# Optimization experiments

Measured on AMD Instinct MI355X. Metric: run time of the kernel, lower is better.

## Reference

```python
import jax, jax.numpy as jnp
import numpy as np

N_NODES = 10000
D_IN = 128
D_OUT = 128
N_EDGES = 640000


def setup_inputs() -> dict:
    key = jax.random.key(0)
    k_x, k_e, k_wl, k_wr, k_b = jax.random.split(key, 5)
    x = jax.random.normal(k_x, (N_NODES, D_IN), dtype=jnp.float32)
    edge_index = jax.random.randint(k_e, (2, N_EDGES), 0, N_NODES, dtype=jnp.int64)
    # SAGEConv params: lin_l (neighbor path, with bias), lin_r (root path, no bias)
    s_l = 1.0 / np.sqrt(D_IN)
    W_l = jax.random.uniform(k_wl, (D_OUT, D_IN), dtype=jnp.float32, minval=-s_l, maxval=s_l)
    b_l = jax.random.uniform(k_b, (D_OUT,), dtype=jnp.float32, minval=-s_l, maxval=s_l)
    W_r = jax.random.uniform(k_wr, (D_OUT, D_IN), dtype=jnp.float32, minval=-s_l, maxval=s_l)
    return {"x": x, "edge_index": edge_index, "W_l": W_l, "b_l": b_l, "W_r": W_r}


def reference(x, edge_index, W_l, b_l, W_r):
    x = x.astype(jnp.float32)
    src, dst = edge_index[0], edge_index[1]
    # gather source features, mean-aggregate into destination nodes
    msgs = x[src]                                   # [E, D_in] irregular gather
    agg_sum = jax.ops.segment_sum(msgs, dst, num_segments=N_NODES)  # [N, D_in]
    deg = jax.ops.segment_sum(jnp.ones((src.shape[0],), dtype=x.dtype), dst,
                              num_segments=N_NODES)                 # [N]
    agg = jnp.where(deg[:, None] > 0, agg_sum / jnp.maximum(deg, 1.0)[:, None], 0.0)
    # SAGEConv: lin_l(agg) + lin_r(x)
    y = agg @ W_l.T + b_l + x @ W_r.T               # [N, D_out]
    return x + y                                     # residual add
```

## Files before the change

### kernel.cpp

```cpp
#include <hip/hip_runtime.h>

#define N_NODES 10000
#define D 128
#define N_EDGES 640000
#define NB 256
#define EPB (N_EDGES / NB)
#define SB 40
#define NPSB 250

typedef __attribute__((ext_vector_type(8))) short bf16x8;
typedef __attribute__((ext_vector_type(4))) float f32x4;
typedef __attribute__((ext_vector_type(8))) unsigned short us8;
typedef __attribute__((ext_vector_type(8))) float f32x8;


__device__ __forceinline__ unsigned short f2bf(float f) {
    union { float f; unsigned int i; } v;
    v.f = f;
    unsigned int b = v.i;
    unsigned int rounded = b + 0x7fffu + ((b >> 16) & 1u);
    return (unsigned short)(rounded >> 16);
}

__device__ __forceinline__ float bf2f(unsigned short u) {
    union { unsigned int i; float f; } v;
    v.i = ((unsigned int)u) << 16;
    return v.f;
}

__device__ __forceinline__ f32x8 bf2f8(us8 v) {
    f32x8 r;
#pragma unroll
    for (int t = 0; t < 8; ++t) r[t] = bf2f(v[t]);
    return r;
}


__global__ __launch_bounds__(1024) void hist_cast_kernel(const int* __restrict__ ei,
                                                         const float4* __restrict__ x4,
                                                         const float4* __restrict__ Wl4,
                                                         const float4* __restrict__ Wr4,
                                                         ushort4* __restrict__ xh4,
                                                         ushort4* __restrict__ Wlb4,
                                                         ushort4* __restrict__ Wrb4,
                                                         unsigned short* __restrict__ lrank,
                                                         unsigned short* __restrict__ cnt,
                                                         unsigned long long* __restrict__ flags) {
    __shared__ int h[N_NODES];
    for (int n = threadIdx.x; n < N_NODES; n += 1024) h[n] = 0;
    if (blockIdx.x == 0 && threadIdx.x < SB) flags[threadIdx.x] = 0ULL;

    const int gid = blockIdx.x * 1024 + threadIdx.x;
    for (int i = gid; i < N_NODES * D / 4; i += NB * 1024) {
        float4 v = x4[i];
        ushort4 o;
        o.x = f2bf(v.x); o.y = f2bf(v.y); o.z = f2bf(v.z); o.w = f2bf(v.w);
        xh4[i] = o;
    }
    if (gid < D * D / 4) {
        float4 a = Wl4[gid], b = Wr4[gid];
        ushort4 oa, ob;
        oa.x = f2bf(a.x); oa.y = f2bf(a.y); oa.z = f2bf(a.z); oa.w = f2bf(a.w);
        ob.x = f2bf(b.x); ob.y = f2bf(b.y); ob.z = f2bf(b.z); ob.w = f2bf(b.w);
        Wlb4[gid] = oa;
        Wrb4[gid] = ob;
    }
    __syncthreads();

    const int base = blockIdx.x * EPB;
    for (int e = base + threadIdx.x; e < base + EPB; e += 1024) {
        int d = ei[N_EDGES + e];
        lrank[e] = (unsigned short)atomicAdd(&h[d], 1);
    }
    __syncthreads();
    unsigned short* c = cnt + (size_t)blockIdx.x * N_NODES;
    for (int n = threadIdx.x; n < N_NODES; n += 1024) c[n] = (unsigned short)h[n];
}


__global__ __launch_bounds__(256) void colscan_scan_kernel(unsigned short* __restrict__ cnt,
                                                           int* __restrict__ row_start,
                                                           unsigned long long* __restrict__ flags) {
    const int t = threadIdx.x;
    const int b = blockIdx.x;
    const int n = b * NPSB + t;
    __shared__ int sc[256];
    __shared__ int blk_excl_sh;

    int deg = 0;
    if (t < NPSB) {
        int s = 0;
#pragma unroll 8
        for (int j = 0; j < NB; ++j) {
            int idx = j * N_NODES + n;
            int v = cnt[idx];
            cnt[idx] = (unsigned short)s;
            s += v;
        }
        deg = s;
    }
    sc[t] = deg;
    __syncthreads();
    for (int off = 1; off < 256; off <<= 1) {
        int v = (t >= off) ? sc[t - off] : 0;
        __syncthreads();
        sc[t] += v;
        __syncthreads();
    }
    const int total = sc[255];
    const int local_excl = sc[t] - deg;

    if (t == 0) {
        int excl = 0;
        if (b == 0) {
            __hip_atomic_store(&flags[0], (2ULL << 32) | (unsigned)total,
                               __ATOMIC_RELEASE, __HIP_MEMORY_SCOPE_AGENT);
        } else {
            __hip_atomic_store(&flags[b], (1ULL << 32) | (unsigned)total,
                               __ATOMIC_RELEASE, __HIP_MEMORY_SCOPE_AGENT);
            int j = b - 1;
            while (j >= 0) {
                unsigned long long f = __hip_atomic_load(&flags[j], __ATOMIC_ACQUIRE,
                                                         __HIP_MEMORY_SCOPE_AGENT);
                unsigned st = (unsigned)(f >> 32);
                if (st == 0) continue;
                excl += (int)(unsigned)(f & 0xffffffffULL);
                if (st == 2) break;
                --j;
            }
            __hip_atomic_store(&flags[b], (2ULL << 32) | (unsigned)(excl + total),
                               __ATOMIC_RELEASE, __HIP_MEMORY_SCOPE_AGENT);
        }
        blk_excl_sh = excl;
    }
    __syncthreads();
    if (t < NPSB) row_start[n] = blk_excl_sh + local_excl;
    if (b == SB - 1 && t == 0) row_start[N_NODES] = N_EDGES;
}


__global__ __launch_bounds__(256) void scatter_kernel(const int* __restrict__ ei,
                                                      const int* __restrict__ row_start,
                                                      const unsigned short* __restrict__ cnt,
                                                      const unsigned short* __restrict__ lrank,
                                                      unsigned short* __restrict__ csr) {
    int i = blockIdx.x * 256 + threadIdx.x;
    if (i < N_EDGES) {
        int b = i / EPB;
        int s = ei[i];
        int d = ei[N_EDGES + i];
        int pos = row_start[d] + (int)cnt[b * N_NODES + d] + (int)lrank[i];
        csr[pos] = (unsigned short)s;
    }
}


__global__ __launch_bounds__(128) void aggregate_kernel(const us8* __restrict__ xh8,
                                                        const int* __restrict__ row_start,
                                                        const unsigned short* __restrict__ csr,
                                                        us8* __restrict__ aggb8) {
    __shared__ f32x8 red[8][16];
    const int node = blockIdx.x;
    const int lane16 = threadIdx.x & 15;
    const int slot = threadIdx.x >> 4;
    const int start = row_start[node];
    const int end = row_start[node + 1];

    f32x8 a0 = 0.f, a1 = 0.f, a2 = 0.f, a3 = 0.f;
    int j = start + slot;
    for (; j + 24 < end; j += 32) {
        int s0 = csr[j], s1 = csr[j + 8], s2 = csr[j + 16], s3 = csr[j + 24];
        us8 v0 = xh8[s0 * 16 + lane16];
        us8 v1 = xh8[s1 * 16 + lane16];
        us8 v2 = xh8[s2 * 16 + lane16];
        us8 v3 = xh8[s3 * 16 + lane16];
        a0 += bf2f8(v0); a1 += bf2f8(v1); a2 += bf2f8(v2); a3 += bf2f8(v3);
    }
    for (; j < end; j += 8) {
        us8 v = xh8[(int)csr[j] * 16 + lane16];
        a0 += bf2f8(v);
    }
    a0 = (a0 + a1) + (a2 + a3);
    red[slot][lane16] = a0;
    __syncthreads();
    if (slot == 0) {
        f32x8 o = red[0][lane16];
#pragma unroll
        for (int s = 1; s < 8; ++s) o += red[s][lane16];
        int cntE = end - start;
        float inv = (cntE > 0) ? 1.0f / (float)cntE : 0.0f;
        us8 pack;
#pragma unroll
        for (int t = 0; t < 8; ++t) pack[t] = f2bf(o[t] * inv);
        aggb8[node * 16 + lane16] = pack;
    }
}


__global__ __launch_bounds__(256) void lin_mfma_kernel(const float* __restrict__ x,
                                                       const unsigned short* __restrict__ aggb,
                                                       const unsigned short* __restrict__ xh,
                                                       const unsigned short* __restrict__ Wlb,
                                                       const unsigned short* __restrict__ Wrb,
                                                       const float* __restrict__ bl,
                                                       float* __restrict__ out) {
    const int wave = threadIdx.x >> 6;
    const int lane = threadIdx.x & 63;
    const int l15 = lane & 15;
    const int quad = lane >> 4;
    const int mt = blockIdx.x * 4 + wave;
    if (mt >= 625) return;
    const int row0 = mt * 16;
    const int out0 = blockIdx.y * 16;

    const int m = row0 + l15;
    const int f = out0 + l15;

    const bf16x8* arow = (const bf16x8*)(aggb + (size_t)m * D) + quad;
    const bf16x8* xrow = (const bf16x8*)(xh   + (size_t)m * D) + quad;
    const bf16x8* wlro = (const bf16x8*)(Wlb + (size_t)f * D) + quad;
    const bf16x8* wrro = (const bf16x8*)(Wrb + (size_t)f * D) + quad;

    f32x4 c = {0.f, 0.f, 0.f, 0.f};
#pragma unroll
    for (int kk = 0; kk < 4; ++kk) {
        c = __builtin_amdgcn_mfma_f32_16x16x32_bf16(arow[kk * 4], wlro[kk * 4], c, 0, 0, 0);
        c = __builtin_amdgcn_mfma_f32_16x16x32_bf16(xrow[kk * 4], wrro[kk * 4], c, 0, 0, 0);
    }

    const float bias = bl[f];
#pragma unroll
    for (int r = 0; r < 4; ++r) {
        int row = row0 + quad * 4 + r;
        int idx = row * D + f;
        out[idx] = x[idx] + bias + c[r];
    }
}

extern "C" void kernel_launch(void* const* d_in, const int* in_sizes, int n_in,
                              void* d_out, int out_size, void* d_ws, size_t ws_size,
                              hipStream_t stream) {
    const float* x  = (const float*)d_in[0];
    const int*   ei = (const int*)d_in[1];
    const float* Wl = (const float*)d_in[2];
    const float* bl = (const float*)d_in[3];
    const float* Wr = (const float*)d_in[4];
    float* out = (float*)d_out;

    unsigned long long* flags = (unsigned long long*)d_ws;
    int* row_start = (int*)(flags + 64);
    unsigned short* cnt   = (unsigned short*)(row_start + 10016);
    unsigned short* lrank = cnt + (size_t)NB * N_NODES;
    unsigned short* csr   = lrank + N_EDGES;
    unsigned short* xh    = csr + N_EDGES;
    unsigned short* aggb  = xh + (size_t)N_NODES * D;
    unsigned short* Wlb   = aggb + (size_t)N_NODES * D;
    unsigned short* Wrb   = Wlb + D * D;

    hist_cast_kernel<<<NB, 1024, 0, stream>>>(ei, (const float4*)x, (const float4*)Wl,
                                              (const float4*)Wr, (ushort4*)xh,
                                              (ushort4*)Wlb, (ushort4*)Wrb,
                                              lrank, cnt, flags);
    colscan_scan_kernel<<<SB, 256, 0, stream>>>(cnt, row_start, flags);
    scatter_kernel<<<(N_EDGES + 255) / 256, 256, 0, stream>>>(ei, row_start, cnt, lrank, csr);
    aggregate_kernel<<<N_NODES, 128, 0, stream>>>((const us8*)xh, row_start, csr,
                                                  (us8*)aggb);
    lin_mfma_kernel<<<dim3(157, 8), 256, 0, stream>>>(x, aggb, xh, Wlb, Wrb, bl, out);
}
```

Baseline: 129.3 us.

## Pack histogram counters in 16-bit halves, halve blocks, use one wave per node in aggregation

The histogram kernel now packs two 16-bit node counters into each 32-bit shared word and uses 128 blocks instead of 256. This halves LDS footprint and init/writeback work, and halves the per-block count matrix the column scan must read. The aggregation kernel maps one 64-lane wave per node, four nodes per block, and reduces across slots with shuffles instead of shared memory and a block barrier. Each node now has 4 slots instead of 8, which lowers per-node memory parallelism. Per-block counts also rise to 5000 edges, which still fits in 16 bits.

```diff
diff --git a/kernel.cpp b/kernel.cpp
--- a/kernel.cpp
+++ b/kernel.cpp
@@ -3,7 +3,7 @@
 #define N_NODES 10000
 #define D 128
 #define N_EDGES 640000
-#define NB 256
+#define NB 128
 #define EPB (N_EDGES / NB)
 #define SB 40
 #define NPSB 250
@@ -46,8 +46,8 @@
                                                          unsigned short* __restrict__ lrank,
                                                          unsigned short* __restrict__ cnt,
                                                          unsigned long long* __restrict__ flags) {
-    __shared__ int h[N_NODES];
-    for (int n = threadIdx.x; n < N_NODES; n += 1024) h[n] = 0;
+    __shared__ unsigned int h[N_NODES / 2];
+    for (int w = threadIdx.x; w < N_NODES / 2; w += 1024) h[w] = 0u;
     if (blockIdx.x == 0 && threadIdx.x < SB) flags[threadIdx.x] = 0ULL;
 
     const int gid = blockIdx.x * 1024 + threadIdx.x;
@@ -70,11 +70,13 @@
     const int base = blockIdx.x * EPB;
     for (int e = base + threadIdx.x; e < base + EPB; e += 1024) {
         int d = ei[N_EDGES + e];
-        lrank[e] = (unsigned short)atomicAdd(&h[d], 1);
-    }
-    __syncthreads();
-    unsigned short* c = cnt + (size_t)blockIdx.x * N_NODES;
-    for (int n = threadIdx.x; n < N_NODES; n += 1024) c[n] = (unsigned short)h[n];
+        int sh = (d & 1) << 4;
+        unsigned int old = atomicAdd(&h[d >> 1], 1u << sh);
+        lrank[e] = (unsigned short)((old >> sh) & 0xffffu);
+    }
+    __syncthreads();
+    unsigned int* c = (unsigned int*)(cnt + (size_t)blockIdx.x * N_NODES);
+    for (int w = threadIdx.x; w < N_NODES / 2; w += 1024) c[w] = h[w];
 }
 
 
@@ -155,43 +157,42 @@
 }
 
 
-__global__ __launch_bounds__(128) void aggregate_kernel(const us8* __restrict__ xh8,
+__global__ __launch_bounds__(256) void aggregate_kernel(const us8* __restrict__ xh8,
                                                         const int* __restrict__ row_start,
                                                         const unsigned short* __restrict__ csr,
                                                         us8* __restrict__ aggb8) {
-    __shared__ f32x8 red[8][16];
-    const int node = blockIdx.x;
-    const int lane16 = threadIdx.x & 15;
-    const int slot = threadIdx.x >> 4;
+    const int node = blockIdx.x * 4 + (threadIdx.x >> 6);
+    const int lane = threadIdx.x & 63;
+    const int lane16 = lane & 15;
+    const int slot = lane >> 4;
     const int start = row_start[node];
     const int end = row_start[node + 1];
 
     f32x8 a0 = 0.f, a1 = 0.f, a2 = 0.f, a3 = 0.f;
     int j = start + slot;
-    for (; j + 24 < end; j += 32) {
-        int s0 = csr[j], s1 = csr[j + 8], s2 = csr[j + 16], s3 = csr[j + 24];
-        us8 v0 = xh8[s0 * 16 + lane16];
-        us8 v1 = xh8[s1 * 16 + lane16];
-        us8 v2 = xh8[s2 * 16 + lane16];
-        us8 v3 = xh8[s3 * 16 + lane16];
-        a0 += bf2f8(v0); a1 += bf2f8(v1); a2 += bf2f8(v2); a3 += bf2f8(v3);
-    }
-    for (; j < end; j += 8) {
-        us8 v = xh8[(int)csr[j] * 16 + lane16];
-        a0 += bf2f8(v);
-    }
+    for (; j + 12 < end; j += 16) {
+        int s0 = csr[j], s1 = csr[j + 4], s2 = csr[j + 8], s3 = csr[j + 12];
+        a0 += bf2f8(xh8[s0 * 16 + lane16]);
+        a1 += bf2f8(xh8[s1 * 16 + lane16]);
+        a2 += bf2f8(xh8[s2 * 16 + lane16]);
+        a3 += bf2f8(xh8[s3 * 16 + lane16]);
+    }
+    for (; j < end; j += 4) a0 += bf2f8(xh8[(int)csr[j] * 16 + lane16]);
     a0 = (a0 + a1) + (a2 + a3);
-    red[slot][lane16] = a0;
-    __syncthreads();
+
+#pragma unroll
+    for (int t = 0; t < 8; ++t) {
+        float v = a0[t];
+        v += __shfl_xor(v, 16, 64);
+        v += __shfl_xor(v, 32, 64);
+        a0[t] = v;
+    }
     if (slot == 0) {
-        f32x8 o = red[0][lane16];
-#pragma unroll
-        for (int s = 1; s < 8; ++s) o += red[s][lane16];
-        int cntE = end - start;
-        float inv = (cntE > 0) ? 1.0f / (float)cntE : 0.0f;
+        int cE = end - start;
+        float inv = (cE > 0) ? 1.0f / (float)cE : 0.0f;
         us8 pack;
 #pragma unroll
-        for (int t = 0; t < 8; ++t) pack[t] = f2bf(o[t] * inv);
+        for (int t = 0; t < 8; ++t) pack[t] = f2bf(a0[t] * inv);
         aggb8[node * 16 + lane16] = pack;
     }
 }
@@ -263,7 +264,7 @@
                                               lrank, cnt, flags);
     colscan_scan_kernel<<<SB, 256, 0, stream>>>(cnt, row_start, flags);
     scatter_kernel<<<(N_EDGES + 255) / 256, 256, 0, stream>>>(ei, row_start, cnt, lrank, csr);
-    aggregate_kernel<<<N_NODES, 128, 0, stream>>>((const us8*)xh, row_start, csr,
-                                                  (us8*)aggb);
+    aggregate_kernel<<<2500, 256, 0, stream>>>((const us8*)xh, row_start, csr,
+                                               (us8*)aggb);
     lin_mfma_kernel<<<dim3(157, 8), 256, 0, stream>>>(x, aggb, xh, Wlb, Wrb, bl, out);
 }
```

After: 121.5 us. -6.1%, faster.
